# Kernel optimization log

Hardware: AMD Instinct MI355X
Metric: run time of the kernel (lower is better)

Reference implementation:

```python
import jax, jax.numpy as jnp
import numpy as np

N, DH, DK, FF = 2048, 256, 64, 32


def setup_inputs() -> dict:
    key = jax.random.key(0)
    ks = jax.random.split(key, 12)
    s = lambda d: 1.0 / np.sqrt(d).astype(np.float32)
    return {
        "x": jax.random.normal(ks[0], (1, N, DH), dtype=jnp.float32),
        "adj": (jax.random.uniform(ks[1], (N, N)) < 0.05).astype(jnp.float32),
        "dense": jax.random.uniform(ks[2], (N, N), dtype=jnp.float32),
        "Wq": jax.random.normal(ks[3], (DH, DK)) * s(DH),
        "bq": jnp.zeros((DK,), jnp.float32),
        "Wk": jax.random.normal(ks[4], (DH, DK)) * s(DH),
        "bk": jnp.zeros((DK,), jnp.float32),
        "Wv": jax.random.normal(ks[5], (DH, DH)) * s(DH),
        "bv": jnp.zeros((DH,), jnp.float32),
        "W1": jax.random.normal(ks[6], (3, FF)) * s(3),
        "b1": jnp.zeros((FF,), jnp.float32),
        "W2": jax.random.normal(ks[7], (FF, FF)) * s(FF),
        "b2": jnp.zeros((FF,), jnp.float32),
        "W3": jax.random.normal(ks[8], (FF, 1)) * s(FF),
        "b3": jnp.zeros((1,), jnp.float32),
    }


def reference(x, adj, dense, Wq, bq, Wk, bk, Wv, bv, W1, b1, W2, b2, W3, b3):
    # x: (1, n, dh). Original repeats x to (n, n, dh); here we exploit that
    # q[i, j] = Q(x_j), k[i, j] = K(x_i), v[i, j] = V(x_j) so no n^2*dh tensor
    # is materialized, while the math is identical.
    x0 = x[0]                      # (n, dh)
    q = x0 @ Wq + bq               # (n, dk), Q(x_j)
    k = x0 @ Wk + bk               # (n, dk), K(x_i)
    v = x0 @ Wv + bv               # (n, dh), V(x_j)
    # out[i, j] = <Q(x_j), K(x_i)>
    scores = k @ q.T               # (n, n)
    feats = jnp.stack((scores, adj, dense), axis=2)      # (n, n, 3)
    h = jax.nn.relu(feats @ W1 + b1)                     # (n, n, FF)
    h = jax.nn.relu(h @ W2 + b2)                         # (n, n, FF)
    focus = jax.nn.softmax((h @ W3 + b3)[..., 0], axis=1)  # (n, n)
    # feature[i] = sum_j focus[i, j] * V(x_j)
    feature = focus @ v            # (n, dh)
    return feature[None]           # (1, n, dh)
```

## Files before the change

### kernel.cpp

```cpp
#include <hip/hip_runtime.h>
#include <math.h>


#define NN  2048
#define DHH 256
#define DKK 64

typedef float    f32x4 __attribute__((ext_vector_type(4)));
typedef _Float16 f16x8 __attribute__((ext_vector_type(8)));
typedef _Float16 f16x4 __attribute__((ext_vector_type(4)));
typedef _Float16 f16x2 __attribute__((ext_vector_type(2)));
typedef int      i32x4 __attribute__((ext_vector_type(4)));

__global__ __launch_bounds__(256) void k_qkv(
    const float* __restrict__ x,
    const float* __restrict__ Wq, const float* __restrict__ bq,
    const float* __restrict__ Wk, const float* __restrict__ bk,
    const float* __restrict__ Wv, const float* __restrict__ bv,
    _Float16* __restrict__ q16, _Float16* __restrict__ k16,
    _Float16* __restrict__ vT)
{
    __shared__ float As[32][64];
    __shared__ float Bs[32][64];
    __shared__ _Float16 Ts[64 * 72];

    const int t  = threadIdx.x;
    const int m0 = blockIdx.x * 64;
    const int yb = blockIdx.y;

    const float* W; const float* bias; int wld; int cw0;
    if (yb == 0)      { W = Wq; bias = bq; wld = 64;  cw0 = 0; }
    else if (yb == 1) { W = Wk; bias = bk; wld = 64;  cw0 = 0; }
    else              { W = Wv; bias = bv; wld = 256; cw0 = (yb - 2) * 64; }

    const int tx = t & 15, ty = t >> 4;
    float acc[4][4] = {};

    for (int k0 = 0; k0 < DHH; k0 += 32) {
        {
            const int rr = t >> 3;
            const int cc = (t & 7) * 4;
            float4 a0 = *(const float4*)(x + (size_t)(m0 + rr)      * DHH + k0 + cc);
            float4 a1 = *(const float4*)(x + (size_t)(m0 + rr + 32) * DHH + k0 + cc);
            As[cc+0][rr]    = a0.x; As[cc+1][rr]    = a0.y; As[cc+2][rr]    = a0.z; As[cc+3][rr]    = a0.w;
            As[cc+0][rr+32] = a1.x; As[cc+1][rr+32] = a1.y; As[cc+2][rr+32] = a1.z; As[cc+3][rr+32] = a1.w;
        }
        {
            const int bk_ = t >> 4;
            const int bc  = (t & 15) * 4;
            *(float4*)&Bs[bk_][bc]      = *(const float4*)(W + (size_t)(k0 + bk_)      * wld + cw0 + bc);
            *(float4*)&Bs[bk_ + 16][bc] = *(const float4*)(W + (size_t)(k0 + bk_ + 16) * wld + cw0 + bc);
        }
        __syncthreads();
        #pragma unroll
        for (int kk = 0; kk < 32; ++kk) {
            float4 a = *(const float4*)&As[kk][ty * 4];
            float4 b = *(const float4*)&Bs[kk][tx * 4];
            float av[4] = {a.x, a.y, a.z, a.w};
            float bw[4] = {b.x, b.y, b.z, b.w};
            #pragma unroll
            for (int ii = 0; ii < 4; ++ii)
                #pragma unroll
                for (int jj = 0; jj < 4; ++jj)
                    acc[ii][jj] = fmaf(av[ii], bw[jj], acc[ii][jj]);
        }
        __syncthreads();
    }

    float4 b4 = *(const float4*)&bias[cw0 + tx * 4];
    float bc4[4] = {b4.x, b4.y, b4.z, b4.w};

    if (yb < 2) {
        _Float16* outp = (yb == 0) ? q16 : k16;
        #pragma unroll
        for (int ii = 0; ii < 4; ++ii) {
            f16x4 hv;
            #pragma unroll
            for (int jj = 0; jj < 4; ++jj) hv[jj] = (_Float16)(acc[ii][jj] + bc4[jj]);
            *(f16x4*)&outp[(size_t)(m0 + ty * 4 + ii) * 64 + tx * 4] = hv;
        }
    } else {
        #pragma unroll
        for (int jj = 0; jj < 4; ++jj) {
            f16x4 hv;
            #pragma unroll
            for (int ii = 0; ii < 4; ++ii) hv[ii] = (_Float16)(acc[ii][jj] + bc4[jj]);
            *(f16x4*)&Ts[(tx * 4 + jj) * 72 + ty * 4] = hv;
        }
        __syncthreads();
        {
            const int c = t >> 2, seg = t & 3;
            f16x8 r0 = *(const f16x8*)&Ts[c * 72 + seg * 16];
            f16x8 r1 = *(const f16x8*)&Ts[c * 72 + seg * 16 + 8];
            *(f16x8*)&vT[(size_t)(cw0 + c) * NN + m0 + seg * 16]     = r0;
            *(f16x8*)&vT[(size_t)(cw0 + c) * NN + m0 + seg * 16 + 8] = r1;
        }
    }
}

__global__ __launch_bounds__(256) void k_scores(
    const _Float16* __restrict__ q16, const _Float16* __restrict__ k16,
    f16x2* __restrict__ schl)
{
    const int t    = threadIdx.x;
    const int lane = t & 63;
    const int w    = t >> 6;
    const int col  = lane & 15;
    const int q    = lane >> 4;

    const int i0 = blockIdx.y * 128 + (w >> 1) * 64;
    const int j0 = blockIdx.x * 128 + (w & 1) * 64;

    f32x4 acc[4][4] = {};

    #pragma unroll
    for (int ks = 0; ks < 2; ++ks) {
        f16x8 a[4], b[4];
        #pragma unroll
        for (int f = 0; f < 4; ++f) {
            a[f] = *(const f16x8*)&k16[(size_t)(i0 + f * 16 + col) * 64 + ks * 32 + q * 8];
            b[f] = *(const f16x8*)&q16[(size_t)(j0 + f * 16 + col) * 64 + ks * 32 + q * 8];
        }
        #pragma unroll
        for (int fm = 0; fm < 4; ++fm)
            #pragma unroll
            for (int fn = 0; fn < 4; ++fn)
                acc[fm][fn] = __builtin_amdgcn_mfma_f32_16x16x32_f16(a[fm], b[fn], acc[fm][fn], 0, 0, 0);
    }

    #pragma unroll
    for (int fm = 0; fm < 4; ++fm)
        #pragma unroll
        for (int fn = 0; fn < 4; ++fn)
            #pragma unroll
            for (int r = 0; r < 4; ++r) {
                const size_t idx = (size_t)(i0 + fm * 16 + q * 4 + r) * NN + j0 + fn * 16 + col;
                const float val = acc[fm][fn][r];
                const _Float16 h = (_Float16)val;
                f16x2 pk; pk[0] = h; pk[1] = (_Float16)(val - (float)h);
                schl[idx] = pk;
            }
}

__global__ __launch_bounds__(256) void k_mlp(
    const f16x2* __restrict__ schl,
    const float* __restrict__ adj, const float* __restrict__ dense,
    const float* __restrict__ W1, const float* __restrict__ b1,
    const float* __restrict__ W2, const float* __restrict__ b2,
    const float* __restrict__ W3,
    _Float16* __restrict__ focus)
{
    __shared__ float red[8];

    const int t    = threadIdx.x;
    const int lane = t & 63;
    const int w    = t >> 6;
    const int col  = lane & 15;
    const int q    = lane >> 4;
    const int i    = blockIdx.x;

    f16x8 w1a0 = {}, w1a1 = {};
    if (q == 0) {
        const float w0a = W1[col],      w0b = W1[col + 16];
        const _Float16 h0a = (_Float16)w0a, h0b = (_Float16)w0b;
        w1a0[0] = h0a; w1a0[1] = h0a;
        w1a0[2] = (_Float16)W1[32 + col];
        w1a0[3] = (_Float16)W1[64 + col];
        w1a0[4] = (_Float16)(w0a - (float)h0a);
        w1a1[0] = h0b; w1a1[1] = h0b;
        w1a1[2] = (_Float16)W1[32 + col + 16];
        w1a1[3] = (_Float16)W1[64 + col + 16];
        w1a1[4] = (_Float16)(w0b - (float)h0b);
    }
    f16x8 w2f0, w2f1;
    #pragma unroll
    for (int j = 0; j < 8; ++j) {
        w2f0[j] = (_Float16)W2[(q * 8 + j) * 32 + col];
        w2f1[j] = (_Float16)W2[(q * 8 + j) * 32 + col + 16];
    }
    f32x4 c1a, c1b, c2a, c2b, w3v, w3v2;
    #pragma unroll
    for (int r = 0; r < 4; ++r) {
        c1a[r]  = b1[q * 4 + r];
        c1b[r]  = b1[16 + q * 4 + r];
        c2a[r]  = b2[q * 4 + r];
        c2b[r]  = b2[16 + q * 4 + r];
        w3v[r]  = W3[q * 4 + r];
        w3v2[r] = W3[16 + q * 4 + r];
    }
    const int idxA = ((2 * q) & 3) * 16 + col;
    const int idxB = ((2 * q + 1) & 3) * 16 + col;
    const bool qlo = (q < 2);

    const f16x2* srow = schl  + (size_t)i * NN;
    const float* arow = adj   + (size_t)i * NN;
    const float* drow = dense + (size_t)i * NN;

    float lg[8];

    for (int c = 0; c < 8; ++c) {
        const int jj = w * 512 + c * 64 + lane;

        const int u_sa = __builtin_bit_cast(int, srow[jj]);
        const int u_ad = __builtin_bit_cast(int,
            __builtin_amdgcn_cvt_pkrtz(arow[jj], drow[jj]));
        const int u_s0 = u_sa & 0xFFFF;

        float lgc = 0.f;
        #pragma unroll
        for (int st = 0; st < 4; ++st) {
            const int src = st * 16 + col;
            int e0 = __shfl(u_sa, src, 64);
            int e1 = __shfl(u_ad, src, 64);
            int e2 = __shfl(u_s0, src, 64);
            if (q != 0) { e0 = 0; e1 = 0; e2 = 0; }
            i32x4 bv = {e0, e1, e2, 0};
            f16x8 B1 = __builtin_bit_cast(f16x8, bv);

            f32x4 hpA = __builtin_amdgcn_mfma_f32_16x16x32_f16(w1a0, B1, c1a, 0, 0, 0);
            f32x4 hpB = __builtin_amdgcn_mfma_f32_16x16x32_f16(w1a1, B1, c1b, 0, 0, 0);

            const int pA0 = __builtin_bit_cast(int, __builtin_amdgcn_cvt_pkrtz(fmaxf(hpA[0], 0.f), fmaxf(hpA[1], 0.f)));
            const int pA1 = __builtin_bit_cast(int, __builtin_amdgcn_cvt_pkrtz(fmaxf(hpA[2], 0.f), fmaxf(hpA[3], 0.f)));
            const int pB0 = __builtin_bit_cast(int, __builtin_amdgcn_cvt_pkrtz(fmaxf(hpB[0], 0.f), fmaxf(hpB[1], 0.f)));
            const int pB1 = __builtin_bit_cast(int, __builtin_amdgcn_cvt_pkrtz(fmaxf(hpB[2], 0.f), fmaxf(hpB[3], 0.f)));

            const int aA0 = __shfl(pA0, idxA, 64);
            const int aA1 = __shfl(pA1, idxA, 64);
            const int aB0 = __shfl(pB0, idxA, 64);
            const int aB1 = __shfl(pB1, idxA, 64);
            const int bA0 = __shfl(pA0, idxB, 64);
            const int bA1 = __shfl(pA1, idxB, 64);
            const int bB0 = __shfl(pB0, idxB, 64);
            const int bB1 = __shfl(pB1, idxB, 64);
            i32x4 b2v = { qlo ? aA0 : aB0, qlo ? aA1 : aB1,
                          qlo ? bA0 : bB0, qlo ? bA1 : bB1 };
            f16x8 B2 = __builtin_bit_cast(f16x8, b2v);

            f32x4 acc0 = __builtin_amdgcn_mfma_f32_16x16x32_f16(w2f0, B2, c2a, 0, 0, 0);
            f32x4 acc1 = __builtin_amdgcn_mfma_f32_16x16x32_f16(w2f1, B2, c2b, 0, 0, 0);

            float p = 0.f;
            #pragma unroll
            for (int r = 0; r < 4; ++r) {
                p = fmaf(fmaxf(acc0[r], 0.f), w3v[r],  p);
                p = fmaf(fmaxf(acc1[r], 0.f), w3v2[r], p);
            }
            p += __shfl_xor(p, 16, 64);
            p += __shfl_xor(p, 32, 64);
            lgc = (q == st) ? p : lgc;
        }
        lg[c] = lgc;
    }

    float lmax = -1e30f;
    #pragma unroll
    for (int u = 0; u < 8; ++u) lmax = fmaxf(lmax, lg[u]);
    #pragma unroll
    for (int off = 32; off > 0; off >>= 1)
        lmax = fmaxf(lmax, __shfl_xor(lmax, off, 64));
    if (lane == 0) red[w] = lmax;
    __syncthreads();
    const float rmax = fmaxf(fmaxf(red[0], red[1]), fmaxf(red[2], red[3]));

    float lsum = 0.f;
    #pragma unroll
    for (int u = 0; u < 8; ++u) { lg[u] = __expf(lg[u] - rmax); lsum += lg[u]; }
    #pragma unroll
    for (int off = 32; off > 0; off >>= 1)
        lsum += __shfl_xor(lsum, off, 64);
    if (lane == 0) red[4 + w] = lsum;
    __syncthreads();
    const float inv = 1.f / (red[4] + red[5] + red[6] + red[7]);

    _Float16* hrow = focus + (size_t)i * 2 * NN;
    const int eb = w * 512 + q * 16 + col;
    #pragma unroll
    for (int u = 0; u < 8; ++u)
        hrow[eb + u * 64] = (_Float16)(lg[u] * inv);
}

__global__ __launch_bounds__(256) void k_feat(
    const _Float16* __restrict__ focus, const _Float16* __restrict__ vT,
    float* __restrict__ out)
{
    __shared__ float rbuf[3][64][8];

    const int t    = threadIdx.x;
    const int lane = t & 63;
    const int w    = t >> 6;
    const int col  = lane & 15;
    const int q    = lane >> 4;

    const int m0 = blockIdx.y * 16;
    const int n0 = blockIdx.x * 32;

    f32x4 acc0 = {}, acc1 = {};

    const size_t arow  = (size_t)(m0 + col) * (2 * NN);
    const size_t brow0 = (size_t)(n0 + col) * NN;
    const size_t brow1 = (size_t)(n0 + 16 + col) * NN;
    const int kb = w * 512 + q * 8;

    #pragma unroll 4
    for (int k0 = 0; k0 < 512; k0 += 32) {
        const int ko = kb + k0;
        f16x8 a  = *(const f16x8*)&focus[arow + ko];
        f16x8 b0 = *(const f16x8*)&vT[brow0 + ko];
        f16x8 b1 = *(const f16x8*)&vT[brow1 + ko];
        acc0 = __builtin_amdgcn_mfma_f32_16x16x32_f16(a, b0, acc0, 0, 0, 0);
        acc1 = __builtin_amdgcn_mfma_f32_16x16x32_f16(a, b1, acc1, 0, 0, 0);
    }

    if (w != 0) {
        *(float4*)&rbuf[w - 1][lane][0] = *(float4*)&acc0;
        *(float4*)&rbuf[w - 1][lane][4] = *(float4*)&acc1;
    }
    __syncthreads();

    if (w == 0) {
        #pragma unroll
        for (int j = 0; j < 3; ++j) {
            float4 p0 = *(const float4*)&rbuf[j][lane][0];
            float4 p1 = *(const float4*)&rbuf[j][lane][4];
            acc0[0] += p0.x; acc0[1] += p0.y; acc0[2] += p0.z; acc0[3] += p0.w;
            acc1[0] += p1.x; acc1[1] += p1.y; acc1[2] += p1.z; acc1[3] += p1.w;
        }
        #pragma unroll
        for (int r = 0; r < 4; ++r) {
            out[(size_t)(m0 + q * 4 + r) * DHH + n0 + col]      = acc0[r];
            out[(size_t)(m0 + q * 4 + r) * DHH + n0 + 16 + col] = acc1[r];
        }
    }
}

extern "C" void kernel_launch(void* const* d_in, const int* in_sizes, int n_in,
                              void* d_out, int out_size, void* d_ws, size_t ws_size,
                              hipStream_t stream) {
    const float* x     = (const float*)d_in[0];
    const float* adj   = (const float*)d_in[1];
    const float* dense = (const float*)d_in[2];
    const float* Wq    = (const float*)d_in[3];
    const float* bq    = (const float*)d_in[4];
    const float* Wk    = (const float*)d_in[5];
    const float* bk    = (const float*)d_in[6];
    const float* Wv    = (const float*)d_in[7];
    const float* bv    = (const float*)d_in[8];
    const float* W1    = (const float*)d_in[9];
    const float* b1    = (const float*)d_in[10];
    const float* W2    = (const float*)d_in[11];
    const float* b2    = (const float*)d_in[12];
    const float* W3    = (const float*)d_in[13];
    float* out = (float*)d_out;

    char* wsb = (char*)d_ws;
    _Float16* q16  = (_Float16*)(wsb);
    _Float16* k16  = (_Float16*)(wsb + 262144);
    _Float16* vT   = (_Float16*)(wsb + 524288);
    f16x2*    schl = (f16x2*)   (wsb + 1572864);
    _Float16* focus= (_Float16*)(wsb + 1572864);

    hipLaunchKernelGGL(k_qkv,    dim3(32, 6),  dim3(256), 0, stream,
                       x, Wq, bq, Wk, bk, Wv, bv, q16, k16, vT);
    hipLaunchKernelGGL(k_scores, dim3(16, 16), dim3(256), 0, stream, q16, k16, schl);
    hipLaunchKernelGGL(k_mlp,    dim3(2048),   dim3(256), 0, stream,
                       schl, adj, dense, W1, b1, W2, b2, W3, focus);
    hipLaunchKernelGGL(k_feat,   dim3(8, 128), dim3(256), 0, stream,
                       focus, vT, out);
}
```

Baseline: 183.6 us.

## Fuse score GEMM into MLP kernel and switch MLP to 16x16x16 MFMAs

Removes the separate k_scores kernel and its 16 MB hi/lo score buffer. Each MLP block now computes its score row on the fly with MFMAs on q16/k16 loaded from cache. The first two MLP layers are also reformulated to use 16x16x16 f16 MFMAs with a different operand layout, which removes most of the cross-lane shuffles. The focus buffer stride shrinks to N. The cost is redundant MFMA work, since each score uses a 16x16 tile but only one column is kept, plus extra q16 loads per edge.

New measurement: 203.0 us. +10.6%, slower.

```diff
diff --git a/kernel.cpp b/kernel.cpp
--- a/kernel.cpp
+++ b/kernel.cpp
@@ -10,7 +10,10 @@
 typedef _Float16 f16x8 __attribute__((ext_vector_type(8)));
 typedef _Float16 f16x4 __attribute__((ext_vector_type(4)));
 typedef _Float16 f16x2 __attribute__((ext_vector_type(2)));
-typedef int      i32x4 __attribute__((ext_vector_type(4)));
+typedef int      i32x2 __attribute__((ext_vector_type(2)));
+
+#define MFMA16(a, b, c) __builtin_amdgcn_mfma_f32_16x16x16f16((a), (b), (c), 0, 0, 0)
+#define MFMA32(a, b, c) __builtin_amdgcn_mfma_f32_16x16x32_f16((a), (b), (c), 0, 0, 0)
 
 __global__ __launch_bounds__(256) void k_qkv(
     const float* __restrict__ x,
@@ -98,52 +101,8 @@
     }
 }
 
-__global__ __launch_bounds__(256) void k_scores(
+__global__ __launch_bounds__(256) void k_mlp(
     const _Float16* __restrict__ q16, const _Float16* __restrict__ k16,
-    f16x2* __restrict__ schl)
-{
-    const int t    = threadIdx.x;
-    const int lane = t & 63;
-    const int w    = t >> 6;
-    const int col  = lane & 15;
-    const int q    = lane >> 4;
-
-    const int i0 = blockIdx.y * 128 + (w >> 1) * 64;
-    const int j0 = blockIdx.x * 128 + (w & 1) * 64;
-
-    f32x4 acc[4][4] = {};
-
-    #pragma unroll
-    for (int ks = 0; ks < 2; ++ks) {
-        f16x8 a[4], b[4];
-        #pragma unroll
-        for (int f = 0; f < 4; ++f) {
-            a[f] = *(const f16x8*)&k16[(size_t)(i0 + f * 16 + col) * 64 + ks * 32 + q * 8];
-            b[f] = *(const f16x8*)&q16[(size_t)(j0 + f * 16 + col) * 64 + ks * 32 + q * 8];
-        }
-        #pragma unroll
-        for (int fm = 0; fm < 4; ++fm)
-            #pragma unroll
-            for (int fn = 0; fn < 4; ++fn)
-                acc[fm][fn] = __builtin_amdgcn_mfma_f32_16x16x32_f16(a[fm], b[fn], acc[fm][fn], 0, 0, 0);
-    }
-
-    #pragma unroll
-    for (int fm = 0; fm < 4; ++fm)
-        #pragma unroll
-        for (int fn = 0; fn < 4; ++fn)
-            #pragma unroll
-            for (int r = 0; r < 4; ++r) {
-                const size_t idx = (size_t)(i0 + fm * 16 + q * 4 + r) * NN + j0 + fn * 16 + col;
-                const float val = acc[fm][fn][r];
-                const _Float16 h = (_Float16)val;
-                f16x2 pk; pk[0] = h; pk[1] = (_Float16)(val - (float)h);
-                schl[idx] = pk;
-            }
-}
-
-__global__ __launch_bounds__(256) void k_mlp(
-    const f16x2* __restrict__ schl,
     const float* __restrict__ adj, const float* __restrict__ dense,
     const float* __restrict__ W1, const float* __restrict__ b1,
     const float* __restrict__ W2, const float* __restrict__ b2,
@@ -159,25 +118,35 @@
     const int q    = lane >> 4;
     const int i    = blockIdx.x;
 
-    f16x8 w1a0 = {}, w1a1 = {};
-    if (q == 0) {
-        const float w0a = W1[col],      w0b = W1[col + 16];
+    const f16x8 kA0 = *(const f16x8*)&k16[(size_t)i * 64 + q * 8];
+    const f16x8 kA1 = *(const f16x8*)&k16[(size_t)i * 64 + 32 + q * 8];
+
+    f16x4 l1A0 = {}, l1A1 = {};
+    {
+        const float w0a = W1[col], w0b = W1[col + 16];
         const _Float16 h0a = (_Float16)w0a, h0b = (_Float16)w0b;
-        w1a0[0] = h0a; w1a0[1] = h0a;
-        w1a0[2] = (_Float16)W1[32 + col];
-        w1a0[3] = (_Float16)W1[64 + col];
-        w1a0[4] = (_Float16)(w0a - (float)h0a);
-        w1a1[0] = h0b; w1a1[1] = h0b;
-        w1a1[2] = (_Float16)W1[32 + col + 16];
-        w1a1[3] = (_Float16)W1[64 + col + 16];
-        w1a1[4] = (_Float16)(w0b - (float)h0b);
-    }
-    f16x8 w2f0, w2f1;
-    #pragma unroll
-    for (int j = 0; j < 8; ++j) {
-        w2f0[j] = (_Float16)W2[(q * 8 + j) * 32 + col];
-        w2f1[j] = (_Float16)W2[(q * 8 + j) * 32 + col + 16];
-    }
+        if (q == 0) {
+            l1A0[0] = h0a; l1A0[1] = h0a;
+            l1A0[2] = (_Float16)W1[32 + col];
+            l1A0[3] = (_Float16)W1[64 + col];
+            l1A1[0] = h0b; l1A1[1] = h0b;
+            l1A1[2] = (_Float16)W1[32 + col + 16];
+            l1A1[3] = (_Float16)W1[64 + col + 16];
+        } else if (q == 1) {
+            l1A0[0] = (_Float16)(w0a - (float)h0a);
+            l1A1[0] = (_Float16)(w0b - (float)h0b);
+        }
+    }
+
+    f16x4 w2A[2][2];
+    #pragma unroll
+    for (int fh = 0; fh < 2; ++fh)
+        #pragma unroll
+        for (int oh = 0; oh < 2; ++oh)
+            #pragma unroll
+            for (int j = 0; j < 4; ++j)
+                w2A[fh][oh][j] = (_Float16)W2[(fh * 16 + q * 4 + j) * 32 + oh * 16 + col];
+
     f32x4 c1a, c1b, c2a, c2b, w3v, w3v2;
     #pragma unroll
     for (int r = 0; r < 4; ++r) {
@@ -188,57 +157,53 @@
         w3v[r]  = W3[q * 4 + r];
         w3v2[r] = W3[16 + q * 4 + r];
     }
-    const int idxA = ((2 * q) & 3) * 16 + col;
-    const int idxB = ((2 * q + 1) & 3) * 16 + col;
-    const bool qlo = (q < 2);
-
-    const f16x2* srow = schl  + (size_t)i * NN;
+
     const float* arow = adj   + (size_t)i * NN;
     const float* drow = dense + (size_t)i * NN;
 
+    const f32x4 zero4 = {0.f, 0.f, 0.f, 0.f};
     float lg[8];
 
     for (int c = 0; c < 8; ++c) {
-        const int jj = w * 512 + c * 64 + lane;
-
-        const int u_sa = __builtin_bit_cast(int, srow[jj]);
+        const int base = w * 512 + c * 64;
+        const int jj   = base + lane;
+
         const int u_ad = __builtin_bit_cast(int,
             __builtin_amdgcn_cvt_pkrtz(arow[jj], drow[jj]));
-        const int u_s0 = u_sa & 0xFFFF;
 
         float lgc = 0.f;
         #pragma unroll
         for (int st = 0; st < 4; ++st) {
-            const int src = st * 16 + col;
-            int e0 = __shfl(u_sa, src, 64);
-            int e1 = __shfl(u_ad, src, 64);
-            int e2 = __shfl(u_s0, src, 64);
-            if (q != 0) { e0 = 0; e1 = 0; e2 = 0; }
-            i32x4 bv = {e0, e1, e2, 0};
-            f16x8 B1 = __builtin_bit_cast(f16x8, bv);
-
-            f32x4 hpA = __builtin_amdgcn_mfma_f32_16x16x32_f16(w1a0, B1, c1a, 0, 0, 0);
-            f32x4 hpB = __builtin_amdgcn_mfma_f32_16x16x32_f16(w1a1, B1, c1b, 0, 0, 0);
-
-            const int pA0 = __builtin_bit_cast(int, __builtin_amdgcn_cvt_pkrtz(fmaxf(hpA[0], 0.f), fmaxf(hpA[1], 0.f)));
-            const int pA1 = __builtin_bit_cast(int, __builtin_amdgcn_cvt_pkrtz(fmaxf(hpA[2], 0.f), fmaxf(hpA[3], 0.f)));
-            const int pB0 = __builtin_bit_cast(int, __builtin_amdgcn_cvt_pkrtz(fmaxf(hpB[0], 0.f), fmaxf(hpB[1], 0.f)));
-            const int pB1 = __builtin_bit_cast(int, __builtin_amdgcn_cvt_pkrtz(fmaxf(hpB[2], 0.f), fmaxf(hpB[3], 0.f)));
-
-            const int aA0 = __shfl(pA0, idxA, 64);
-            const int aA1 = __shfl(pA1, idxA, 64);
-            const int aB0 = __shfl(pB0, idxA, 64);
-            const int aB1 = __shfl(pB1, idxA, 64);
-            const int bA0 = __shfl(pA0, idxB, 64);
-            const int bA1 = __shfl(pA1, idxB, 64);
-            const int bB0 = __shfl(pB0, idxB, 64);
-            const int bB1 = __shfl(pB1, idxB, 64);
-            i32x4 b2v = { qlo ? aA0 : aB0, qlo ? aA1 : aB1,
-                          qlo ? bA0 : bB0, qlo ? bA1 : bB1 };
-            f16x8 B2 = __builtin_bit_cast(f16x8, b2v);
-
-            f32x4 acc0 = __builtin_amdgcn_mfma_f32_16x16x32_f16(w2f0, B2, c2a, 0, 0, 0);
-            f32x4 acc1 = __builtin_amdgcn_mfma_f32_16x16x32_f16(w2f1, B2, c2b, 0, 0, 0);
+            const int edge = base + st * 16 + col;
+
+            f16x8 Qb0 = *(const f16x8*)&q16[(size_t)edge * 64 + q * 8];
+            f16x8 Qb1 = *(const f16x8*)&q16[(size_t)edge * 64 + 32 + q * 8];
+            f32x4 sC = MFMA32(kA0, Qb0, zero4);
+            sC = MFMA32(kA1, Qb1, sC);
+            const float s = sC[0];
+
+            const _Float16 shi = (_Float16)s;
+            _Float16 slo = (_Float16)(s - (float)shi);
+            if (q == 1) slo = (_Float16)0;
+            f16x2 r0; r0[0] = shi; r0[1] = slo;
+            const int ad = __shfl(u_ad, st * 16 + col, 64);
+            i32x2 b1v = { __builtin_bit_cast(int, r0), ad };
+            f16x4 B1 = __builtin_bit_cast(f16x4, b1v);
+
+            f32x4 hpA = MFMA16(l1A0, B1, c1a);
+            f32x4 hpB = MFMA16(l1A1, B1, c1b);
+
+            i32x2 p0 = { __builtin_bit_cast(int, __builtin_amdgcn_cvt_pkrtz(fmaxf(hpA[0], 0.f), fmaxf(hpA[1], 0.f))),
+                         __builtin_bit_cast(int, __builtin_amdgcn_cvt_pkrtz(fmaxf(hpA[2], 0.f), fmaxf(hpA[3], 0.f))) };
+            i32x2 p1 = { __builtin_bit_cast(int, __builtin_amdgcn_cvt_pkrtz(fmaxf(hpB[0], 0.f), fmaxf(hpB[1], 0.f))),
+                         __builtin_bit_cast(int, __builtin_amdgcn_cvt_pkrtz(fmaxf(hpB[2], 0.f), fmaxf(hpB[3], 0.f))) };
+            f16x4 B2f0 = __builtin_bit_cast(f16x4, p0);
+            f16x4 B2f1 = __builtin_bit_cast(f16x4, p1);
+
+            f32x4 acc0 = MFMA16(w2A[0][0], B2f0, c2a);
+            acc0 = MFMA16(w2A[1][0], B2f1, acc0);
+            f32x4 acc1 = MFMA16(w2A[0][1], B2f0, c2b);
+            acc1 = MFMA16(w2A[1][1], B2f1, acc1);
 
             float p = 0.f;
             #pragma unroll
@@ -273,7 +238,7 @@
     __syncthreads();
     const float inv = 1.f / (red[4] + red[5] + red[6] + red[7]);
 
-    _Float16* hrow = focus + (size_t)i * 2 * NN;
+    _Float16* hrow = focus + (size_t)i * NN;
     const int eb = w * 512 + q * 16 + col;
     #pragma unroll
     for (int u = 0; u < 8; ++u)
@@ -297,7 +262,7 @@
 
     f32x4 acc0 = {}, acc1 = {};
 
-    const size_t arow  = (size_t)(m0 + col) * (2 * NN);
+    const size_t arow  = (size_t)(m0 + col) * NN;
     const size_t brow0 = (size_t)(n0 + col) * NN;
     const size_t brow1 = (size_t)(n0 + 16 + col) * NN;
     const int kb = w * 512 + q * 8;
@@ -308,8 +273,8 @@
         f16x8 a  = *(const f16x8*)&focus[arow + ko];
         f16x8 b0 = *(const f16x8*)&vT[brow0 + ko];
         f16x8 b1 = *(const f16x8*)&vT[brow1 + ko];
-        acc0 = __builtin_amdgcn_mfma_f32_16x16x32_f16(a, b0, acc0, 0, 0, 0);
-        acc1 = __builtin_amdgcn_mfma_f32_16x16x32_f16(a, b1, acc1, 0, 0, 0);
+        acc0 = MFMA32(a, b0, acc0);
+        acc1 = MFMA32(a, b1, acc1);
     }
 
     if (w != 0) {
@@ -354,17 +319,15 @@
     float* out = (float*)d_out;
 
     char* wsb = (char*)d_ws;
-    _Float16* q16  = (_Float16*)(wsb);
-    _Float16* k16  = (_Float16*)(wsb + 262144);
-    _Float16* vT   = (_Float16*)(wsb + 524288);
-    f16x2*    schl = (f16x2*)   (wsb + 1572864);
-    _Float16* focus= (_Float16*)(wsb + 1572864);
-
-    hipLaunchKernelGGL(k_qkv,    dim3(32, 6),  dim3(256), 0, stream,
+    _Float16* q16   = (_Float16*)(wsb);
+    _Float16* k16   = (_Float16*)(wsb + 262144);
+    _Float16* vT    = (_Float16*)(wsb + 524288);
+    _Float16* focus = (_Float16*)(wsb + 1572864);
+
+    hipLaunchKernelGGL(k_qkv,  dim3(32, 6),  dim3(256), 0, stream,
                        x, Wq, bq, Wk, bk, Wv, bv, q16, k16, vT);
-    hipLaunchKernelGGL(k_scores, dim3(16, 16), dim3(256), 0, stream, q16, k16, schl);
-    hipLaunchKernelGGL(k_mlp,    dim3(2048),   dim3(256), 0, stream,
-                       schl, adj, dense, W1, b1, W2, b2, W3, focus);
-    hipLaunchKernelGGL(k_feat,   dim3(8, 128), dim3(256), 0, stream,
+    hipLaunchKernelGGL(k_mlp,  dim3(2048),   dim3(256), 0, stream,
+                       q16, k16, adj, dense, W1, b1, W2, b2, W3, focus);
+    hipLaunchKernelGGL(k_feat, dim3(8, 128), dim3(256), 0, stream,
                        focus, vT, out);
 }
```
